# Performance work log

Hardware: AMD Instinct MI355X
Metric: run time of the kernel (lower is better)

Reference implementation:

```python
import jax, jax.numpy as jnp
import numpy as np
from jax import lax

BINS = 16
N_FFT = 2 * (BINS - 1)  # 30


def setup_inputs() -> dict:
    key = jax.random.key(0)
    k0, k1, k2, k3 = jax.random.split(key, 4)
    B, C, T = 16, 256, 8192
    c = C // BINS  # 16
    s = 1.0 / np.sqrt(C)  # keep attention logits in a sane range
    return {
        "x": jax.random.normal(k0, (B, C, T), dtype=jnp.float32),
        "Wk": jax.random.normal(k1, (c, C), dtype=jnp.float32) * s,
        "Wq": jax.random.normal(k2, (C, C), dtype=jnp.float32) * s,
        "Wv": jax.random.normal(k3, (C, C), dtype=jnp.float32) * s,
    }


def _spectrogram_power(sig):
    """torchaudio T.Spectrogram(n_fft=30, hop_length=1, normalized=True, power=2),
    implemented as a direct windowed-DFT conv (exact same math as the FFT).
    sig: [N, L] -> [N, BINS, L+1] frames (center=True, reflect pad)."""
    n = jnp.arange(N_FFT, dtype=jnp.float32)
    window = 0.5 - 0.5 * jnp.cos(2.0 * np.pi * n / N_FFT)  # periodic Hann
    kf = jnp.arange(BINS, dtype=jnp.float32)
    ang = 2.0 * np.pi * kf[:, None] * n[None, :] / N_FFT  # [BINS, N_FFT]
    # real and imaginary DFT kernels, window folded in: [2*BINS, N_FFT]
    dft = jnp.concatenate([jnp.cos(ang), -jnp.sin(ang)], axis=0) * window
    pad = N_FFT // 2
    sigp = jnp.pad(sig, ((0, 0), (pad, pad)), mode="reflect")[:, None, :]  # [N,1,L+30]
    spec = lax.conv_general_dilated(
        sigp, dft[:, None, :].astype(sig.dtype), (1,), "VALID",
        dimension_numbers=("NCH", "OIH", "NCH"))  # [N, 2*BINS, L+1]
    power = spec[:, :BINS, :] ** 2 + spec[:, BINS:, :] ** 2
    return power / jnp.sum(window ** 2)  # normalized=True -> / ||w||^2 on power


def reference(x, Wk, Wq, Wv):
    B, C, T = x.shape
    c = Wk.shape[0]
    xt = x.transpose(0, 2, 1)  # [B, T, C]
    k = jnp.einsum("btC,cC->bct", xt, Wk)   # [B, c, T]
    q = jnp.einsum("btC,cC->bct", xt, Wq)   # [B, C, T]
    v = jnp.einsum("btC,cC->bct", xt, Wv)   # [B, C, T]
    scores = jnp.einsum("bct,bCt->bcC", k, q) / (C ** 0.5)
    scores = jax.nn.softmax(scores, axis=-1)           # [B, c, C]
    out = jnp.einsum("bCt,bcC->bct", v, scores)        # [B, c, T]
    power = _spectrogram_power(out.reshape(B * c, T))  # [B*c, BINS, T+1]
    power = power[..., :T]                             # drop last frame ([:-1])
    return power.reshape(B, c * BINS, T)
```

## Files before the change

### kernel.cpp

```cpp
#include <hip/hip_runtime.h>
#include <math.h>

#define B_   16
#define C_   256
#define T_   8192
#define BINS 16
#define NFFT 30

typedef __attribute__((ext_vector_type(8))) _Float16 f16x8;
typedef __attribute__((ext_vector_type(2))) __fp16 fp16x2;
typedef __attribute__((ext_vector_type(4))) float f32x4;

typedef const __attribute__((address_space(1))) unsigned int ga_u32;
typedef __attribute__((address_space(3))) unsigned int ls_u32;

union f16pack { f16x8 v; fp16x2 p[4]; };

__global__ __launch_bounds__(256) void k_kernel(const float* __restrict__ x,
                                                const float* __restrict__ Wk,
                                                _Float16* __restrict__ kk) {
  const int tc = blockIdx.x;
  const int b  = blockIdx.y;
  const int tid = threadIdx.x;
  const int t = tc*512 + tid*2;
  const float* xb = x + (size_t)b*C_*T_ + t;
  float2 acc[16];
#pragma unroll
  for (int cc = 0; cc < 16; ++cc) acc[cc] = make_float2(0.f, 0.f);
  for (int c4 = 0; c4 < 64; ++c4) {
    float2 xv[4];
#pragma unroll
    for (int j = 0; j < 4; ++j) xv[j] = *(const float2*)(xb + (size_t)(c4*4 + j)*T_);
#pragma unroll
    for (int cc = 0; cc < 16; ++cc) {
      const float4 w4 = *(const float4*)&Wk[cc*256 + c4*4];
      acc[cc].x += w4.x*xv[0].x + w4.y*xv[1].x + w4.z*xv[2].x + w4.w*xv[3].x;
      acc[cc].y += w4.x*xv[0].y + w4.y*xv[1].y + w4.z*xv[2].y + w4.w*xv[3].y;
    }
  }
#pragma unroll
  for (int cc = 0; cc < 16; ++cc) {
    fp16x2 hv;
    hv[0] = (__fp16)acc[cc].x;
    hv[1] = (__fp16)acc[cc].y;
    *(fp16x2*)&kk[((size_t)b*16 + cc)*T_ + t] = hv;
  }
}

static __device__ __forceinline__ void stage_panel(float* dstbase, const float* xb,
                                                   int koff, int tid) {
#pragma unroll
  for (int h = 0; h < 4; ++h) {
    const int idx = h*512 + tid;
    const int row = idx >> 3;
    const int ps  = idx & 7;
    const int ls  = ps ^ (row & 7);
    const float* src = xb + (size_t)row*T_ + koff + ls*4;
    __builtin_amdgcn_global_load_lds((ga_u32*)src, (ls_u32*)(dstbase + idx*4), 16, 0, 0);
  }
}

__global__ __launch_bounds__(512, 4) void r_kernel(const float* __restrict__ x,
                                                   const _Float16* __restrict__ kk,
                                                   float* __restrict__ Rp) {
  const int ks = blockIdx.x;
  const int b  = blockIdx.y;
  constexpr int KCH = 256;

  __shared__ float P[2][256*32];

  const int tid  = threadIdx.x;
  const int lane = tid & 63;
  const int w    = tid >> 6;
  const int fr   = lane & 15;
  const int g    = lane >> 4;

  const float* xb = x + (size_t)b*C_*T_;
  const _Float16* kb = kk + (size_t)b*16*T_;
  const int t0 = ks * KCH;

  f32x4 acc[2];
  acc[0] = (f32x4){0.f,0.f,0.f,0.f};
  acc[1] = (f32x4){0.f,0.f,0.f,0.f};

  stage_panel(P[0], xb, t0, tid);
  __syncthreads();

  int cur = 0;
  for (int kt = 0; kt < KCH; kt += 32) {
    if (kt + 32 < KCH) stage_panel(P[cur ^ 1], xb, t0 + kt + 32, tid);

    const float* Pc = P[cur];
    const f16x8 ka = *(const f16x8*)&kb[(size_t)fr*T_ + t0 + kt + g*8];
#pragma unroll
    for (int nt = 0; nt < 2; ++nt) {
      const int r = (w*2 + nt)*16 + fr;
      const float4 lo = *(const float4*)&Pc[r*32 + (((2*g+0) ^ (r&7))<<2)];
      const float4 hi = *(const float4*)&Pc[r*32 + (((2*g+1) ^ (r&7))<<2)];
      f16pack fb;
      fb.p[0] = __builtin_amdgcn_cvt_pkrtz(lo.x, lo.y);
      fb.p[1] = __builtin_amdgcn_cvt_pkrtz(lo.z, lo.w);
      fb.p[2] = __builtin_amdgcn_cvt_pkrtz(hi.x, hi.y);
      fb.p[3] = __builtin_amdgcn_cvt_pkrtz(hi.z, hi.w);
      acc[nt] = __builtin_amdgcn_mfma_f32_16x16x32_f16(ka, fb.v, acc[nt], 0, 0, 0);
    }
    __syncthreads();
    cur ^= 1;
  }

  float* rp = Rp + ((size_t)(ks*16 + b))*4096;
#pragma unroll
  for (int nt = 0; nt < 2; ++nt)
#pragma unroll
    for (int r = 0; r < 4; ++r) {
      const int cc = g*4 + r;
      const int ch = (w*2 + nt)*16 + fr;
      rp[cc*256 + ch] = acc[nt][r];
    }
}

__global__ __launch_bounds__(256) void reduce_kernel(const float* __restrict__ Rp,
                                                     float* __restrict__ wkg) {
  const int idx = blockIdx.x*256 + threadIdx.x;
  const int b   = idx >> 12;
  const int rem = idx & 4095;
  float s = 0.f;
#pragma unroll 8
  for (int p = 0; p < 32; ++p)
    s += Rp[((size_t)(p*16 + b))*4096 + rem];
  wkg[idx] = s;
}

__global__ __launch_bounds__(512) void attn_b(const float* __restrict__ Wq,
                                              const float* __restrict__ Wv,
                                              const float* __restrict__ wkg,
                                              float* __restrict__ Mout) {
  const int b = blockIdx.x;
  const int tid = threadIdx.x;
  __shared__ float s1[16*256];
  __shared__ float s2[16*256];
  __shared__ float invs[16];

  for (int i = tid; i < 4096; i += 512) s1[i] = wkg[(size_t)b*4096 + i];
  __syncthreads();

  const int h   = tid >> 8;
  const int col = tid & 255;

  float sc[8];
#pragma unroll
  for (int i = 0; i < 8; ++i) sc[i] = 0.f;
  for (int c4 = 0; c4 < 64; ++c4) {
    const float4 wq4 = *(const float4*)&Wq[(size_t)col*256 + c4*4];
#pragma unroll
    for (int i = 0; i < 8; ++i) {
      const float4 p4 = *(const float4*)&s1[(h*8 + i)*256 + c4*4];
      sc[i] += p4.x*wq4.x + p4.y*wq4.y + p4.z*wq4.z + p4.w*wq4.w;
    }
  }
#pragma unroll
  for (int i = 0; i < 8; ++i) s2[(h*8 + i)*256 + col] = sc[i] * 0.0625f;
  __syncthreads();

  {
    const int rr = tid >> 5, jj = tid & 31;
    float mx = -1e30f;
    for (int c = jj; c < 256; c += 32) mx = fmaxf(mx, s2[rr*256 + c]);
#pragma unroll
    for (int o = 1; o < 32; o <<= 1) mx = fmaxf(mx, __shfl_xor(mx, o, 64));
    float sm = 0.f;
    for (int c = jj; c < 256; c += 32) {
      const float e = __expf(s2[rr*256 + c] - mx);
      s2[rr*256 + c] = e;
      sm += e;
    }
#pragma unroll
    for (int o = 1; o < 32; o <<= 1) sm += __shfl_xor(sm, o, 64);
    if (jj == 0) invs[rr] = 1.f / sm;
  }
  __syncthreads();

  float mac[8];
#pragma unroll
  for (int i = 0; i < 8; ++i) mac[i] = 0.f;
  for (int c4 = 0; c4 < 64; ++c4) {
    float wv[4];
#pragma unroll
    for (int j = 0; j < 4; ++j) wv[j] = Wv[(size_t)(c4*4 + j)*256 + col];
#pragma unroll
    for (int i = 0; i < 8; ++i) {
      const float4 p4 = *(const float4*)&s2[(h*8 + i)*256 + c4*4];
      mac[i] += p4.x*wv[0] + p4.y*wv[1] + p4.z*wv[2] + p4.w*wv[3];
    }
  }
#pragma unroll
  for (int i = 0; i < 8; ++i)
    Mout[(size_t)b*4096 + (h*8 + i)*256 + col] = mac[i] * invs[h*8 + i];
}

__global__ __launch_bounds__(256) void outp_kernel(const float* __restrict__ x,
                                                   const float* __restrict__ M,
                                                   float* __restrict__ seq) {
  const int tc = blockIdx.x;
  const int b  = blockIdx.y;
  const int tid = threadIdx.x;
  const int t  = tc*512 + tid*2;
  const float* xb = x + (size_t)b*C_*T_ + t;
  const float* mb = M + (size_t)b*4096;
  float2 a[16];
#pragma unroll
  for (int cc = 0; cc < 16; ++cc) a[cc] = make_float2(0.f, 0.f);
  for (int ch = 0; ch < 64; ++ch) {
    float2 xv[4];
#pragma unroll
    for (int j = 0; j < 4; ++j)
      xv[j] = *(const float2*)(xb + (size_t)(ch*4 + j) * T_);
#pragma unroll
    for (int cc = 0; cc < 16; ++cc) {
      const float4 m4 = *(const float4*)(mb + cc*256 + ch*4);
      a[cc].x += m4.x*xv[0].x + m4.y*xv[1].x + m4.z*xv[2].x + m4.w*xv[3].x;
      a[cc].y += m4.x*xv[0].y + m4.y*xv[1].y + m4.z*xv[2].y + m4.w*xv[3].y;
    }
  }
#pragma unroll
  for (int cc = 0; cc < 16; ++cc)
    *(float2*)(seq + (size_t)(b*16 + cc)*T_ + t) = a[cc];
}

__global__ __launch_bounds__(256) void spec_kernel(const float* __restrict__ seq,
                                                   float* __restrict__ out) {
  const int tcx = blockIdx.x;
  const int r   = blockIdx.y;
  const int tid = threadIdx.x;
  const int t0  = tcx * 256;

  __shared__ float smem[288];
  __shared__ float ctab[BINS*NFFT];
  __shared__ float stab[BINS*NFFT];

  const float* row = seq + (size_t)r * T_;
  for (int i = tid; i < 288; i += 256) {
    int gg = t0 - 15 + i;
    if (gg < 0) gg = -gg;
    if (gg > T_-1) gg = 2*(T_-1) - gg;
    smem[i] = row[gg];
  }
  for (int i = tid; i < BINS*NFFT; i += 256) {
    const int k = i / NFFT, n = i % NFFT;
    const float TWO_PI = 6.283185307179586f;
    const float wn = 0.5f - 0.5f * cosf(TWO_PI * (float)n / (float)NFFT);
    const float ang = TWO_PI * (float)(k * n) / (float)NFFT;
    ctab[i] = cosf(ang) * wn;
    stab[i] = sinf(ang) * wn;
  }
  __syncthreads();

  const int k   = tid >> 4;
  const int sub = tid & 15;
  float cr[NFFT], ci[NFFT];
#pragma unroll
  for (int n = 0; n < NFFT; ++n) { cr[n] = ctab[k*NFFT + n]; ci[n] = stab[k*NFFT + n]; }

  float* orow = out + (size_t)(r*BINS + k) * T_ + t0;
  const float inv_norm = 1.0f / 11.25f;

  for (int jj = 0; jj < 4; ++jj) {
    const int x0 = 4*sub + 64*jj;
    float smp[36];
#pragma unroll
    for (int q = 0; q < 9; ++q) {
      const float4 v = *(const float4*)&smem[x0 + 4*q];
      smp[4*q+0] = v.x; smp[4*q+1] = v.y; smp[4*q+2] = v.z; smp[4*q+3] = v.w;
    }
    float4 pw;
#pragma unroll
    for (int p = 0; p < 4; ++p) {
      float re = 0.f, im = 0.f;
#pragma unroll
      for (int n = 0; n < NFFT; ++n) {
        re += cr[n] * smp[p + n];
        im += ci[n] * smp[p + n];
      }
      ((float*)&pw)[p] = (re*re + im*im) * inv_norm;
    }
    *(float4*)(orow + x0) = pw;
  }
}

extern "C" void kernel_launch(void* const* d_in, const int* in_sizes, int n_in,
                              void* d_out, int out_size, void* d_ws, size_t ws_size,
                              hipStream_t stream) {
  const float* x  = (const float*)d_in[0];
  const float* Wk = (const float*)d_in[1];
  const float* Wq = (const float*)d_in[2];
  const float* Wv = (const float*)d_in[3];
  float* out = (float*)d_out;
  float* ws  = (float*)d_ws;

  _Float16* kk = (_Float16*)ws;
  float* Rp   = ws + 1048576;
  float* wkg  = Rp + 2097152;
  float* M    = wkg + 65536;
  float* seq  = M + 65536;

  k_kernel<<<dim3(16, 16), 256, 0, stream>>>(x, Wk, kk);
  r_kernel<<<dim3(32, 16), 512, 0, stream>>>(x, kk, Rp);
  reduce_kernel<<<dim3(256), 256, 0, stream>>>(Rp, wkg);
  attn_b<<<dim3(16), 512, 0, stream>>>(Wq, Wv, wkg, M);
  outp_kernel<<<dim3(16, 16), 256, 0, stream>>>(x, M, seq);
  spec_kernel<<<dim3(32, 256), 256, 0, stream>>>(seq, out);
}
```

Before: 213.5 us.

## Fuse output projection into spectrogram kernel, recomputing halo samples in shared memory

Merges the output projection (M·x) with the spectrogram kernel. Each block computes 288 time samples (256 plus a 30-sample reflect halo) for 8 output channels directly from x into shared memory, then runs the DFT on them. This removes the intermediate seq buffer round-trip through global memory and one kernel launch. In exchange, x is re-read once per channel half (2x across blocks), the halo is recomputed by neighbouring blocks, and only 1024 blocks launch, each doing serial work over 8 channels.

```diff
diff --git a/kernel.cpp b/kernel.cpp
--- a/kernel.cpp
+++ b/kernel.cpp
@@ -198,52 +198,25 @@
     Mout[(size_t)b*4096 + (h*8 + i)*256 + col] = mac[i] * invs[h*8 + i];
 }
 
-__global__ __launch_bounds__(256) void outp_kernel(const float* __restrict__ x,
-                                                   const float* __restrict__ M,
-                                                   float* __restrict__ seq) {
-  const int tc = blockIdx.x;
-  const int b  = blockIdx.y;
-  const int tid = threadIdx.x;
-  const int t  = tc*512 + tid*2;
-  const float* xb = x + (size_t)b*C_*T_ + t;
-  const float* mb = M + (size_t)b*4096;
-  float2 a[16];
-#pragma unroll
-  for (int cc = 0; cc < 16; ++cc) a[cc] = make_float2(0.f, 0.f);
-  for (int ch = 0; ch < 64; ++ch) {
-    float2 xv[4];
-#pragma unroll
-    for (int j = 0; j < 4; ++j)
-      xv[j] = *(const float2*)(xb + (size_t)(ch*4 + j) * T_);
-#pragma unroll
-    for (int cc = 0; cc < 16; ++cc) {
-      const float4 m4 = *(const float4*)(mb + cc*256 + ch*4);
-      a[cc].x += m4.x*xv[0].x + m4.y*xv[1].x + m4.z*xv[2].x + m4.w*xv[3].x;
-      a[cc].y += m4.x*xv[0].y + m4.y*xv[1].y + m4.z*xv[2].y + m4.w*xv[3].y;
-    }
-  }
-#pragma unroll
-  for (int cc = 0; cc < 16; ++cc)
-    *(float2*)(seq + (size_t)(b*16 + cc)*T_ + t) = a[cc];
-}
-
-__global__ __launch_bounds__(256) void spec_kernel(const float* __restrict__ seq,
-                                                   float* __restrict__ out) {
+#define SLP 292
+
+__global__ __launch_bounds__(256) void outspec(const float* __restrict__ x,
+                                               const float* __restrict__ M,
+                                               float* __restrict__ out) {
   const int tcx = blockIdx.x;
-  const int r   = blockIdx.y;
+  const int b   = blockIdx.y;
+  const int hf  = blockIdx.z;
   const int tid = threadIdx.x;
   const int t0  = tcx * 256;
 
-  __shared__ float smem[288];
+  __shared__ float Mt[256*8];
+  __shared__ float sl[8*SLP];
   __shared__ float ctab[BINS*NFFT];
   __shared__ float stab[BINS*NFFT];
 
-  const float* row = seq + (size_t)r * T_;
-  for (int i = tid; i < 288; i += 256) {
-    int gg = t0 - 15 + i;
-    if (gg < 0) gg = -gg;
-    if (gg > T_-1) gg = 2*(T_-1) - gg;
-    smem[i] = row[gg];
+  for (int i = tid; i < 2048; i += 256) {
+    const int ch = i >> 3, c = i & 7;
+    Mt[ch*8 + c] = M[(size_t)b*4096 + (hf*8 + c)*256 + ch];
   }
   for (int i = tid; i < BINS*NFFT; i += 256) {
     const int k = i / NFFT, n = i % NFFT;
@@ -255,35 +228,69 @@
   }
   __syncthreads();
 
+  const float* xb = x + (size_t)b*C_*T_;
+#pragma unroll
+  for (int pass = 0; pass < 2; ++pass) {
+    const int i = pass*256 + tid;
+    if (i < 288) {
+      int t = t0 - 15 + i;
+      if (t < 0) t = -t;
+      if (t > T_-1) t = 2*(T_-1) - t;
+      float acc[8];
+#pragma unroll
+      for (int c = 0; c < 8; ++c) acc[c] = 0.f;
+      for (int c4 = 0; c4 < 64; ++c4) {
+        float xv[4];
+#pragma unroll
+        for (int j = 0; j < 4; ++j) xv[j] = xb[(size_t)(c4*4 + j)*T_ + t];
+#pragma unroll
+        for (int j = 0; j < 4; ++j) {
+          const float4 m0 = *(const float4*)&Mt[(c4*4 + j)*8];
+          const float4 m1 = *(const float4*)&Mt[(c4*4 + j)*8 + 4];
+          acc[0] += xv[j]*m0.x; acc[1] += xv[j]*m0.y;
+          acc[2] += xv[j]*m0.z; acc[3] += xv[j]*m0.w;
+          acc[4] += xv[j]*m1.x; acc[5] += xv[j]*m1.y;
+          acc[6] += xv[j]*m1.z; acc[7] += xv[j]*m1.w;
+        }
+      }
+#pragma unroll
+      for (int c = 0; c < 8; ++c) sl[c*SLP + i] = acc[c];
+    }
+  }
+  __syncthreads();
+
   const int k   = tid >> 4;
   const int sub = tid & 15;
   float cr[NFFT], ci[NFFT];
 #pragma unroll
   for (int n = 0; n < NFFT; ++n) { cr[n] = ctab[k*NFFT + n]; ci[n] = stab[k*NFFT + n]; }
 
-  float* orow = out + (size_t)(r*BINS + k) * T_ + t0;
   const float inv_norm = 1.0f / 11.25f;
-
-  for (int jj = 0; jj < 4; ++jj) {
-    const int x0 = 4*sub + 64*jj;
-    float smp[36];
-#pragma unroll
-    for (int q = 0; q < 9; ++q) {
-      const float4 v = *(const float4*)&smem[x0 + 4*q];
-      smp[4*q+0] = v.x; smp[4*q+1] = v.y; smp[4*q+2] = v.z; smp[4*q+3] = v.w;
-    }
-    float4 pw;
-#pragma unroll
-    for (int p = 0; p < 4; ++p) {
-      float re = 0.f, im = 0.f;
-#pragma unroll
-      for (int n = 0; n < NFFT; ++n) {
-        re += cr[n] * smp[p + n];
-        im += ci[n] * smp[p + n];
+  for (int c = 0; c < 8; ++c) {
+    const float* row = &sl[c*SLP];
+    float* orow = out + (((size_t)(b*16 + hf*8 + c))*BINS + k)*T_ + t0;
+#pragma unroll
+    for (int jj = 0; jj < 4; ++jj) {
+      const int x0 = 4*sub + 64*jj;
+      float smp[36];
+#pragma unroll
+      for (int q = 0; q < 9; ++q) {
+        const float4 v = *(const float4*)&row[x0 + 4*q];
+        smp[4*q+0] = v.x; smp[4*q+1] = v.y; smp[4*q+2] = v.z; smp[4*q+3] = v.w;
       }
-      ((float*)&pw)[p] = (re*re + im*im) * inv_norm;
-    }
-    *(float4*)(orow + x0) = pw;
+      float4 pw;
+#pragma unroll
+      for (int p = 0; p < 4; ++p) {
+        float re = 0.f, im = 0.f;
+#pragma unroll
+        for (int n = 0; n < NFFT; ++n) {
+          re += cr[n] * smp[p + n];
+          im += ci[n] * smp[p + n];
+        }
+        ((float*)&pw)[p] = (re*re + im*im) * inv_norm;
+      }
+      *(float4*)(orow + x0) = pw;
+    }
   }
 }
 
@@ -301,12 +308,10 @@
   float* Rp   = ws + 1048576;
   float* wkg  = Rp + 2097152;
   float* M    = wkg + 65536;
-  float* seq  = M + 65536;
 
   k_kernel<<<dim3(16, 16), 256, 0, stream>>>(x, Wk, kk);
   r_kernel<<<dim3(32, 16), 512, 0, stream>>>(x, kk, Rp);
   reduce_kernel<<<dim3(256), 256, 0, stream>>>(Rp, wkg);
   attn_b<<<dim3(16), 512, 0, stream>>>(Wq, Wv, wkg, M);
-  outp_kernel<<<dim3(16, 16), 256, 0, stream>>>(x, M, seq);
-  spec_kernel<<<dim3(32, 256), 256, 0, stream>>>(seq, out);
-}
+  outspec<<<dim3(32, 16, 2), 256, 0, stream>>>(x, M, out);
+}
```

Result: slower. 240.0 us (+12.4%).
